# Kernel optimization log

Hardware: AMD Instinct MI355X
Metric: run time of the kernel (lower is better)

## Reference

```python
import jax, jax.numpy as jnp
import numpy as np

D_MODEL = 1024
H = 16
DH = 64
EPS = 1e-5


def _layernorm(x, g, b):
    mu = jnp.mean(x, axis=-1, keepdims=True)
    var = jnp.var(x, axis=-1, keepdims=True)
    return (x - mu) * jax.lax.rsqrt(var + EPS) * g + b


def setup_inputs() -> dict:
    key = jax.random.key(0)
    ks = jax.random.split(key, 16)
    B, L = 4, 4096
    s = 0.02
    inp = {
        "x": jax.random.normal(ks[0], (B, L, D_MODEL), jnp.float32),
        "ln1_g": jnp.ones((D_MODEL,), jnp.float32),
        "ln1_b": jnp.zeros((D_MODEL,), jnp.float32),
        "Wq": jax.random.normal(ks[1], (D_MODEL, H * DH), jnp.float32) * s,
        "bq": jnp.zeros((H * DH,), jnp.float32),
        "Wk": jax.random.normal(ks[2], (D_MODEL, H * DH), jnp.float32) * s,
        "bk": jnp.zeros((H * DH,), jnp.float32),
        "Wv": jax.random.normal(ks[3], (D_MODEL, H * DH), jnp.float32) * s,
        "bv": jnp.zeros((H * DH,), jnp.float32),
        "Wg": jax.random.normal(ks[4], (D_MODEL, H * DH), jnp.float32) * s,
        "bg": jnp.zeros((H * DH,), jnp.float32),
        "decay_logit": jnp.zeros((H,), jnp.float32),
        "Wo": jax.random.normal(ks[5], (H * DH, D_MODEL), jnp.float32) * s,
        "bo": jnp.zeros((D_MODEL,), jnp.float32),
        "ln2_g": jnp.ones((D_MODEL,), jnp.float32),
        "ln2_b": jnp.zeros((D_MODEL,), jnp.float32),
        "W1": jax.random.normal(ks[6], (D_MODEL, 4 * D_MODEL), jnp.float32) * s,
        "b1": jnp.zeros((4 * D_MODEL,), jnp.float32),
        "W2": jax.random.normal(ks[7], (4 * D_MODEL, D_MODEL), jnp.float32) * s,
        "b2": jnp.zeros((D_MODEL,), jnp.float32),
    }
    return inp


def reference(x, ln1_g, ln1_b, Wq, bq, Wk, bk, Wv, bv, Wg, bg, decay_logit,
              Wo, bo, ln2_g, ln2_b, W1, b1, W2, b2):
    B, L, _ = x.shape
    y = _layernorm(x, ln1_g, ln1_b)
    # projections -> [L, B, H, DH] (time-major for scan)
    def proj(W, b):
        return (y @ W + b).reshape(B, L, H, DH).transpose(1, 0, 2, 3)
    q = proj(Wq, bq)
    k = proj(Wk, bk)
    v = proj(Wv, bv)
    g = jax.nn.sigmoid(y @ Wg + bg).reshape(B, L, H, DH).transpose(1, 0, 2, 3)
    decay = jax.nn.sigmoid(decay_logit)[None, :, None]  # [1,H,1]
    scale = DH ** -0.5

    def step(state, qkvg):
        q_t, k_t, v_t, g_t = qkvg
        state = decay * state + k_t * v_t          # [B,H,DH]
        out_t = g_t * q_t * state * scale
        return state, out_t

    state0 = jnp.zeros((B, H, DH), x.dtype)
    _, outs = jax.lax.scan(step, state0, (q, k, v, g))  # [L,B,H,DH]
    o = outs.transpose(1, 0, 2, 3).reshape(B, L, H * DH) @ Wo + bo
    x2 = x + o  # dropout is identity (eval / p=0)
    h = _layernorm(x2, ln2_g, ln2_b)
    ff = jax.nn.gelu(h @ W1 + b1, approximate=False) @ W2 + b2
    return x2 + ff
```

## Files before the change

### kernel.cpp

```cpp
#include <hip/hip_runtime.h>
#include <math.h>


#define D_MODEL 1024
#define LSEQ    4096
#define BATCH   4
#define NROWS   (BATCH * LSEQ)
#define HEADS   16
#define DH      64
#define CHUNK   128
#define NCH     (LSEQ / CHUNK)

typedef short  short8  __attribute__((ext_vector_type(8)));
typedef short  short4v __attribute__((ext_vector_type(4)));
typedef float  float4v __attribute__((ext_vector_type(4)));

__device__ inline short f2bf(float f) {
    unsigned u = __float_as_uint(f);
    u += 0x7fffu + ((u >> 16) & 1u);
    return (short)(u >> 16);
}
__device__ inline float bf2f(short s) {
    return __uint_as_float(((unsigned)(unsigned short)s) << 16);
}

__device__ inline void load_lds16(const short* g, short* l) {
    __builtin_amdgcn_global_load_lds(
        (const __attribute__((address_space(1))) void*)g,
        (__attribute__((address_space(3))) void*)l,
        16, 0, 0);
}

__global__ __launch_bounds__(1024) void transpose_f32_bf16(
    const float* __restrict__ in, short* __restrict__ out, int R, int C)
{
    __shared__ float tile[32][33];
    int tx = threadIdx.x, ty = threadIdx.y;
    int r = blockIdx.y * 32 + ty;
    int c = blockIdx.x * 32 + tx;
    tile[ty][tx] = in[(size_t)r * C + c];
    __syncthreads();
    out[(size_t)(blockIdx.x * 32 + ty) * R + blockIdx.y * 32 + tx] =
        f2bf(tile[tx][ty]);
}

__global__ __launch_bounds__(256) void concat_bias(
    const float* __restrict__ bq, const float* __restrict__ bk,
    const float* __restrict__ bv, const float* __restrict__ bg,
    float* __restrict__ out)
{
    int i = blockIdx.x * 256 + threadIdx.x;
    const float* src = (i < 1024) ? bq : (i < 2048) ? bk : (i < 3072) ? bv : bg;
    out[i] = src[i & 1023];
}

__global__ __launch_bounds__(256) void ln_kernel(
    const float* __restrict__ x, const float* __restrict__ g,
    const float* __restrict__ b, short* __restrict__ y)
{
    int row = blockIdx.x;
    int tid = threadIdx.x;
    const float4* xr = (const float4*)(x + (size_t)row * D_MODEL);
    float4 v = xr[tid];
    float s  = v.x + v.y + v.z + v.w;
    float ss = v.x * v.x + v.y * v.y + v.z * v.z + v.w * v.w;
    #pragma unroll
    for (int off = 32; off > 0; off >>= 1) {
        s  += __shfl_down(s, off);
        ss += __shfl_down(ss, off);
    }
    __shared__ float sbuf[8];
    int wv = tid >> 6, ln = tid & 63;
    if (ln == 0) { sbuf[wv] = s; sbuf[4 + wv] = ss; }
    __syncthreads();
    float tot  = sbuf[0] + sbuf[1] + sbuf[2] + sbuf[3];
    float tot2 = sbuf[4] + sbuf[5] + sbuf[6] + sbuf[7];
    float mu  = tot * (1.0f / D_MODEL);
    float var = tot2 * (1.0f / D_MODEL) - mu * mu;
    float rs  = rsqrtf(var + 1e-5f);
    float4 gg = ((const float4*)g)[tid];
    float4 bb = ((const float4*)b)[tid];
    short4v o;
    o.x = f2bf((v.x - mu) * rs * gg.x + bb.x);
    o.y = f2bf((v.y - mu) * rs * gg.y + bb.y);
    o.z = f2bf((v.z - mu) * rs * gg.z + bb.z);
    o.w = f2bf((v.w - mu) * rs * gg.w + bb.w);
    ((short4v*)y)[(size_t)row * 256 + tid] = o;
}

__global__ __launch_bounds__(512, 2) void gemm_bf16(
    const short* __restrict__ A, const short* __restrict__ BT,
    const float* __restrict__ bias, const float* __restrict__ res,
    float* __restrict__ outf, short* __restrict__ outb,
    int M, int N, int K, int mode)
{
    __shared__ short As[2][16384];
    __shared__ short Bs[2][16384];

    const int gx  = gridDim.x;
    const int nwg = gx * gridDim.y;
    const int lin = blockIdx.x + blockIdx.y * gx;
    const int cpx = nwg >> 3;
    const int wg  = (lin & 7) * cpx + (lin >> 3);
    const int bx  = wg % gx;
    const int by  = wg / gx;
    const int row0 = bx * 256;
    const int col0 = by * 256;

    const int tid  = threadIdx.x;
    const int wave = tid >> 6;
    const int lane = tid & 63;
    const int wm   = wave >> 2;
    const int wn   = wave & 3;
    const int lm   = lane & 15;
    const int q    = lane >> 4;
    const int kq0  = ((q ^ (lm & 7)) << 3);

    const int csw = (((tid & 7) ^ ((tid >> 3) & 7)) << 3);
    const short* gA = A  + (size_t)(row0 + (tid >> 3)) * K + csw;
    const short* gB = BT + (size_t)(col0 + (tid >> 3)) * K + csw;
    short* sA = &As[0][0] + tid * 8;
    short* sB = &Bs[0][0] + tid * 8;
    const size_t K64 = (size_t)64 * K;

    float4v acc[8][4];
    #pragma unroll
    for (int i = 0; i < 8; i++)
        #pragma unroll
        for (int j = 0; j < 4; j++)
            acc[i][j] = (float4v)(0.0f);

    const int NT = K >> 6;

    load_lds16(gA,            sA);
    load_lds16(gA +     K64,  sA + 4096);
    load_lds16(gA + 2 * K64,  sA + 8192);
    load_lds16(gA + 3 * K64,  sA + 12288);
    load_lds16(gB,            sB);
    load_lds16(gB +     K64,  sB + 4096);
    load_lds16(gB + 2 * K64,  sB + 8192);
    load_lds16(gB + 3 * K64,  sB + 12288);
    __syncthreads();

    const short* Abase = &As[0][0] + wm * 8192;
    const short* Bbase = &Bs[0][0] + (wn >> 1) * 8192;
    const int aro = lm * 64;
    const int bro = ((wn & 1) * 64 + lm) * 64;

    short8 aF[4][2];
    short8 bF[2][2][2];

#define MFMA8(QR, QC)                                                        \
    _Pragma("unroll")                                                        \
    for (int ks = 0; ks < 2; ks++)                                           \
        _Pragma("unroll")                                                    \
        for (int i = 0; i < 4; i++)                                          \
            _Pragma("unroll")                                                \
            for (int j = 0; j < 2; j++)                                      \
                acc[(QR) * 4 + i][(QC) * 2 + j] =                            \
                    __builtin_amdgcn_mfma_f32_16x16x32_bf16(                 \
                        aF[i][ks], bF[QC][j][ks],                            \
                        acc[(QR) * 4 + i][(QC) * 2 + j], 0, 0, 0);

    for (int t = 0; t < NT; ++t) {
        const int bufo = (t & 1) << 14;
        const short* Ab = Abase + bufo;
        const short* Bb = Bbase + bufo;
        const int  kb = (t + 1) << 6;
        const bool pf = (t + 1 < NT);
        const int  pfo = ((t + 1) & 1) << 14;

        #pragma unroll
        for (int i = 0; i < 4; i++) {
            const int ar = aro + (i * 16) * 64;
            aF[i][0] = *(const short8*)&Ab[ar + kq0];
            aF[i][1] = *(const short8*)&Ab[ar + (kq0 ^ 32)];
        }
        #pragma unroll
        for (int j = 0; j < 2; j++) {
            const int br = bro + (j * 16) * 64;
            bF[0][j][0] = *(const short8*)&Bb[br + kq0];
            bF[0][j][1] = *(const short8*)&Bb[br + (kq0 ^ 32)];
        }
        if (pf) {
            short* d = sA + pfo;
            load_lds16(gA + kb,            d);
            load_lds16(gA +     K64 + kb,  d + 4096);
            load_lds16(gA + 2 * K64 + kb,  d + 8192);
            load_lds16(gA + 3 * K64 + kb,  d + 12288);
        }
        __builtin_amdgcn_s_barrier();
        __builtin_amdgcn_s_setprio(1);
        MFMA8(0, 0)
        __builtin_amdgcn_s_setprio(0);
        __builtin_amdgcn_s_barrier();

        #pragma unroll
        for (int j = 0; j < 2; j++) {
            const int br = bro + (32 + j * 16) * 64;
            bF[1][j][0] = *(const short8*)&Bb[br + kq0];
            bF[1][j][1] = *(const short8*)&Bb[br + (kq0 ^ 32)];
        }
        if (pf) {
            short* d = sB + pfo;
            load_lds16(gB + kb,            d);
            load_lds16(gB +     K64 + kb,  d + 4096);
            load_lds16(gB + 2 * K64 + kb,  d + 8192);
            load_lds16(gB + 3 * K64 + kb,  d + 12288);
        }
        __builtin_amdgcn_s_barrier();
        __builtin_amdgcn_s_setprio(1);
        MFMA8(0, 1)
        __builtin_amdgcn_s_setprio(0);
        __builtin_amdgcn_s_barrier();

        #pragma unroll
        for (int i = 0; i < 4; i++) {
            const int ar = aro + (64 + i * 16) * 64;
            aF[i][0] = *(const short8*)&Ab[ar + kq0];
            aF[i][1] = *(const short8*)&Ab[ar + (kq0 ^ 32)];
        }
        __builtin_amdgcn_s_barrier();
        __builtin_amdgcn_s_setprio(1);
        MFMA8(1, 0)
        __builtin_amdgcn_s_setprio(0);
        __builtin_amdgcn_s_barrier();

        __builtin_amdgcn_s_setprio(1);
        MFMA8(1, 1)
        __builtin_amdgcn_s_setprio(0);
        __syncthreads();
    }
#undef MFMA8

    const int r4 = q << 2;
    #pragma unroll
    for (int ai = 0; ai < 8; ai++) {
        const int rowg = row0 + wm * 128 + (ai >> 2) * 64 + (ai & 3) * 16 + r4;
        #pragma unroll
        for (int bj = 0; bj < 4; bj++) {
            const int colg = col0 + wn * 64 + (bj >> 1) * 32 + (bj & 1) * 16 + lm;
            const float bcol = bias[colg];
            #pragma unroll
            for (int r2 = 0; r2 < 4; r2++) {
                size_t idx = (size_t)(rowg + r2) * N + colg;
                float v = acc[ai][bj][r2] + bcol;
                if (mode == 0) {
                    if (colg >= 3072) v = 1.0f / (1.0f + expf(-v));
                    outb[idx] = f2bf(v);
                } else if (mode == 1) {
                    outf[idx] = v + res[idx];
                } else {
                    v = 0.5f * v * (1.0f + erff(v * 0.70710678118654752f));
                    outb[idx] = f2bf(v);
                }
            }
        }
    }
}

__global__ __launch_bounds__(256) void scan_pass1(
    const short* __restrict__ qkvg, const float* __restrict__ dlogit,
    float* __restrict__ carry)
{
    int j  = blockIdx.x >> 4;
    int c  = ((blockIdx.x & 15) << 8) + threadIdx.x;
    int b  = c >> 10;
    int col = c & 1023;
    float decay = 1.0f / (1.0f + expf(-dlogit[col >> 6]));
    size_t base = ((size_t)b * LSEQ + j * CHUNK) * 4096 + col;
    float s = 0.0f;
    for (int t = 0; t < CHUNK; ++t) {
        float kk = bf2f(qkvg[base + 1024]);
        float vv = bf2f(qkvg[base + 2048]);
        s = decay * s + kk * vv;
        base += 4096;
    }
    carry[j * 4096 + c] = s;
}

__global__ __launch_bounds__(256) void scan_combine(
    const float* __restrict__ carry, const float* __restrict__ dlogit,
    float* __restrict__ sinit)
{
    int c = blockIdx.x * 256 + threadIdx.x;
    float decay = 1.0f / (1.0f + expf(-dlogit[(c & 1023) >> 6]));
    float dp = powf(decay, (float)CHUNK);
    float s = 0.0f;
    for (int j = 0; j < NCH; ++j) {
        sinit[j * 4096 + c] = s;
        s = dp * s + carry[j * 4096 + c];
    }
}

__global__ __launch_bounds__(256) void scan_pass2(
    const short* __restrict__ qkvg, const float* __restrict__ dlogit,
    const float* __restrict__ sinit, short* __restrict__ att)
{
    int j  = blockIdx.x >> 4;
    int c  = ((blockIdx.x & 15) << 8) + threadIdx.x;
    int b  = c >> 10;
    int col = c & 1023;
    float decay = 1.0f / (1.0f + expf(-dlogit[col >> 6]));
    float s = sinit[j * 4096 + c];
    size_t base  = ((size_t)b * LSEQ + j * CHUNK) * 4096 + col;
    size_t obase = ((size_t)b * LSEQ + j * CHUNK) * 1024 + col;
    for (int t = 0; t < CHUNK; ++t) {
        float qq = bf2f(qkvg[base]);
        float kk = bf2f(qkvg[base + 1024]);
        float vv = bf2f(qkvg[base + 2048]);
        float gg = bf2f(qkvg[base + 3072]);
        s = decay * s + kk * vv;
        att[obase] = f2bf(gg * qq * s * 0.125f);
        base += 4096; obase += 1024;
    }
}

extern "C" void kernel_launch(void* const* d_in, const int* in_sizes, int n_in,
                              void* d_out, int out_size, void* d_ws, size_t ws_size,
                              hipStream_t stream)
{
    const float* x      = (const float*)d_in[0];
    const float* ln1_g  = (const float*)d_in[1];
    const float* ln1_b  = (const float*)d_in[2];
    const float* Wq     = (const float*)d_in[3];
    const float* bq     = (const float*)d_in[4];
    const float* Wk     = (const float*)d_in[5];
    const float* bk     = (const float*)d_in[6];
    const float* Wv     = (const float*)d_in[7];
    const float* bv     = (const float*)d_in[8];
    const float* Wg     = (const float*)d_in[9];
    const float* bg     = (const float*)d_in[10];
    const float* dlog   = (const float*)d_in[11];
    const float* Wo     = (const float*)d_in[12];
    const float* bo     = (const float*)d_in[13];
    const float* ln2_g  = (const float*)d_in[14];
    const float* ln2_b  = (const float*)d_in[15];
    const float* W1     = (const float*)d_in[16];
    const float* b1     = (const float*)d_in[17];
    const float* W2     = (const float*)d_in[18];
    const float* b2     = (const float*)d_in[19];
    float* out = (float*)d_out;

    char* ws = (char*)d_ws;
    size_t off = 0;
    auto alloc = [&](size_t bytes) -> void* {
        void* p = ws + off;
        off += (bytes + 255) & ~(size_t)255;
        return p;
    };
    short* WqkvgT = (short*)alloc((size_t)4096 * 1024 * 2);
    short* WoT    = (short*)alloc((size_t)1024 * 1024 * 2);
    short* W1T    = (short*)alloc((size_t)4096 * 1024 * 2);
    short* W2T    = (short*)alloc((size_t)1024 * 4096 * 2);
    float* biasq  = (float*)alloc((size_t)4096 * 4);
    float* carry  = (float*)alloc((size_t)NCH * 4096 * 4);
    float* sinit  = (float*)alloc((size_t)NCH * 4096 * 4);
    short* bufA   = (short*)alloc((size_t)NROWS * 1024 * 2);
    short* bufB   = (short*)alloc((size_t)NROWS * 4096 * 2);
    float* x2 = out;
    short* ybuf = bufA;
    short* att  = bufA;
    short* hbuf = bufA;
    short* qkvg = bufB;
    short* ff1  = bufB;
    (void)in_sizes; (void)n_in; (void)out_size;

    if (off > ws_size) return;

    dim3 tb(32, 32);
    transpose_f32_bf16<<<dim3(32, 32), tb, 0, stream>>>(Wq, WqkvgT + 0 * 1024 * 1024, 1024, 1024);
    transpose_f32_bf16<<<dim3(32, 32), tb, 0, stream>>>(Wk, WqkvgT + 1 * 1024 * 1024, 1024, 1024);
    transpose_f32_bf16<<<dim3(32, 32), tb, 0, stream>>>(Wv, WqkvgT + 2 * 1024 * 1024, 1024, 1024);
    transpose_f32_bf16<<<dim3(32, 32), tb, 0, stream>>>(Wg, WqkvgT + 3 * 1024 * 1024, 1024, 1024);
    transpose_f32_bf16<<<dim3(32, 32), tb, 0, stream>>>(Wo, WoT, 1024, 1024);
    transpose_f32_bf16<<<dim3(128, 32), tb, 0, stream>>>(W1, W1T, 1024, 4096);
    transpose_f32_bf16<<<dim3(32, 128), tb, 0, stream>>>(W2, W2T, 4096, 1024);
    concat_bias<<<16, 256, 0, stream>>>(bq, bk, bv, bg, biasq);

    ln_kernel<<<NROWS, 256, 0, stream>>>(x, ln1_g, ln1_b, ybuf);

    gemm_bf16<<<dim3(64, 16), 512, 0, stream>>>(
        ybuf, WqkvgT, biasq, nullptr, nullptr, qkvg, NROWS, 4096, 1024, 0);

    scan_pass1 <<<NCH * 16, 256, 0, stream>>>(qkvg, dlog, carry);
    scan_combine<<<16, 256, 0, stream>>>(carry, dlog, sinit);
    scan_pass2 <<<NCH * 16, 256, 0, stream>>>(qkvg, dlog, sinit, att);

    gemm_bf16<<<dim3(64, 4), 512, 0, stream>>>(
        att, WoT, bo, x, x2, nullptr, NROWS, 1024, 1024, 1);

    ln_kernel<<<NROWS, 256, 0, stream>>>(x2, ln2_g, ln2_b, hbuf);

    gemm_bf16<<<dim3(64, 16), 512, 0, stream>>>(
        hbuf, W1T, b1, nullptr, nullptr, ff1, NROWS, 4096, 1024, 2);

    gemm_bf16<<<dim3(64, 4), 512, 0, stream>>>(
        ff1, W2T, b2, x2, out, nullptr, NROWS, 1024, 4096, 1);
}
```

Baseline: 1.034 ms.

## Issue next-tile LDS prefetch at loop top with explicit vmcnt waits

The GEMM main loop now issues all eight global-to-LDS loads for the next K tile at the start of each iteration. It then waits with a partial s_waitcnt vmcnt(8), so only the current tile's loads must have landed, and drops the full __syncthreads at the top and end of the loop. This is meant to give the loads more time in flight and replace the heavyweight syncs with a raw s_barrier. It depends on exact vmcnt counting and on the existing mid-loop barriers keeping the double buffer safe, so any other outstanding vector memory op could break correctness.

New measurement: 1.167 ms. +12.8%, slower.

```diff
diff --git a/kernel.cpp b/kernel.cpp
--- a/kernel.cpp
+++ b/kernel.cpp
@@ -140,7 +140,6 @@
     load_lds16(gB +     K64,  sB + 4096);
     load_lds16(gB + 2 * K64,  sB + 8192);
     load_lds16(gB + 3 * K64,  sB + 12288);
-    __syncthreads();
 
     const short* Abase = &As[0][0] + wm * 8192;
     const short* Bbase = &Bs[0][0] + (wn >> 1) * 8192;
@@ -166,9 +165,29 @@
         const int bufo = (t & 1) << 14;
         const short* Ab = Abase + bufo;
         const short* Bb = Bbase + bufo;
-        const int  kb = (t + 1) << 6;
-        const bool pf = (t + 1 < NT);
-        const int  pfo = ((t + 1) & 1) << 14;
+
+        if (t + 1 < NT) {
+            const int kb  = (t + 1) << 6;
+            const int pfo = ((t + 1) & 1) << 14;
+            short* dA = sA + pfo;
+            short* dB = sB + pfo;
+            load_lds16(gA + kb,            dA);
+            load_lds16(gA +     K64 + kb,  dA + 4096);
+            load_lds16(gA + 2 * K64 + kb,  dA + 8192);
+            load_lds16(gA + 3 * K64 + kb,  dA + 12288);
+            load_lds16(gB + kb,            dB);
+            load_lds16(gB +     K64 + kb,  dB + 4096);
+            load_lds16(gB + 2 * K64 + kb,  dB + 8192);
+            load_lds16(gB + 3 * K64 + kb,  dB + 12288);
+            __builtin_amdgcn_sched_barrier(0);
+            asm volatile("s_waitcnt vmcnt(8)" ::: "memory");
+        } else {
+            __builtin_amdgcn_sched_barrier(0);
+            asm volatile("s_waitcnt vmcnt(0)" ::: "memory");
+        }
+        __builtin_amdgcn_sched_barrier(0);
+        __builtin_amdgcn_s_barrier();
+        __builtin_amdgcn_sched_barrier(0);
 
         #pragma unroll
         for (int i = 0; i < 4; i++) {
@@ -182,13 +201,6 @@
             bF[0][j][0] = *(const short8*)&Bb[br + kq0];
             bF[0][j][1] = *(const short8*)&Bb[br + (kq0 ^ 32)];
         }
-        if (pf) {
-            short* d = sA + pfo;
-            load_lds16(gA + kb,            d);
-            load_lds16(gA +     K64 + kb,  d + 4096);
-            load_lds16(gA + 2 * K64 + kb,  d + 8192);
-            load_lds16(gA + 3 * K64 + kb,  d + 12288);
-        }
         __builtin_amdgcn_s_barrier();
         __builtin_amdgcn_s_setprio(1);
         MFMA8(0, 0)
@@ -201,13 +213,6 @@
             bF[1][j][0] = *(const short8*)&Bb[br + kq0];
             bF[1][j][1] = *(const short8*)&Bb[br + (kq0 ^ 32)];
         }
-        if (pf) {
-            short* d = sB + pfo;
-            load_lds16(gB + kb,            d);
-            load_lds16(gB +     K64 + kb,  d + 4096);
-            load_lds16(gB + 2 * K64 + kb,  d + 8192);
-            load_lds16(gB + 3 * K64 + kb,  d + 12288);
-        }
         __builtin_amdgcn_s_barrier();
         __builtin_amdgcn_s_setprio(1);
         MFMA8(0, 1)
@@ -229,7 +234,6 @@
         __builtin_amdgcn_s_setprio(1);
         MFMA8(1, 1)
         __builtin_amdgcn_s_setprio(0);
-        __syncthreads();
     }
 #undef MFMA8
 
```

## Deepen GEMM global-to-LDS prefetch to two tiles ahead with fine-grained vmcnt waits

Applied to the files above, without the earlier changes.

Restructures the bf16 GEMM main loop so global-to-LDS loads are issued up to two K-tiles ahead. Each quarter-buffer is refilled as soon as its MFMA phase has consumed it, and explicit s_waitcnt vmcnt counts replace the full __syncthreads at the end of each iteration. The loop is unrolled by two over the double buffer. This is meant to hide more global latency and remove the end-of-iteration full-barrier stall. The cost is more in-flight loads, a subtler buffer-reuse ordering, and a loop that assumes NT is even.

New measurement: 1.563 ms. +51.1%, slower.

```diff
diff --git a/kernel.cpp b/kernel.cpp
--- a/kernel.cpp
+++ b/kernel.cpp
@@ -119,8 +119,8 @@
     const int csw = (((tid & 7) ^ ((tid >> 3) & 7)) << 3);
     const short* gA = A  + (size_t)(row0 + (tid >> 3)) * K + csw;
     const short* gB = BT + (size_t)(col0 + (tid >> 3)) * K + csw;
-    short* sA = &As[0][0] + tid * 8;
-    short* sB = &Bs[0][0] + tid * 8;
+    short* stA = &As[0][0] + tid * 8;
+    short* stB = &Bs[0][0] + tid * 8;
     const size_t K64 = (size_t)64 * K;
 
     float4v acc[8][4];
@@ -132,18 +132,6 @@
 
     const int NT = K >> 6;
 
-    load_lds16(gA,            sA);
-    load_lds16(gA +     K64,  sA + 4096);
-    load_lds16(gA + 2 * K64,  sA + 8192);
-    load_lds16(gA + 3 * K64,  sA + 12288);
-    load_lds16(gB,            sB);
-    load_lds16(gB +     K64,  sB + 4096);
-    load_lds16(gB + 2 * K64,  sB + 8192);
-    load_lds16(gB + 3 * K64,  sB + 12288);
-    __syncthreads();
-
-    const short* Abase = &As[0][0] + wm * 8192;
-    const short* Bbase = &Bs[0][0] + (wn >> 1) * 8192;
     const int aro = lm * 64;
     const int bro = ((wn & 1) * 64 + lm) * 64;
 
@@ -162,76 +150,94 @@
                         aF[i][ks], bF[QC][j][ks],                            \
                         acc[(QR) * 4 + i][(QC) * 2 + j], 0, 0, 0);
 
-    for (int t = 0; t < NT; ++t) {
-        const int bufo = (t & 1) << 14;
-        const short* Ab = Abase + bufo;
-        const short* Bb = Bbase + bufo;
-        const int  kb = (t + 1) << 6;
-        const bool pf = (t + 1 < NT);
-        const int  pfo = ((t + 1) & 1) << 14;
-
-        #pragma unroll
-        for (int i = 0; i < 4; i++) {
-            const int ar = aro + (i * 16) * 64;
-            aF[i][0] = *(const short8*)&Ab[ar + kq0];
-            aF[i][1] = *(const short8*)&Ab[ar + (kq0 ^ 32)];
-        }
-        #pragma unroll
-        for (int j = 0; j < 2; j++) {
-            const int br = bro + (j * 16) * 64;
-            bF[0][j][0] = *(const short8*)&Bb[br + kq0];
-            bF[0][j][1] = *(const short8*)&Bb[br + (kq0 ^ 32)];
-        }
-        if (pf) {
-            short* d = sA + pfo;
-            load_lds16(gA + kb,            d);
-            load_lds16(gA +     K64 + kb,  d + 4096);
-            load_lds16(gA + 2 * K64 + kb,  d + 8192);
-            load_lds16(gA + 3 * K64 + kb,  d + 12288);
-        }
-        __builtin_amdgcn_s_barrier();
-        __builtin_amdgcn_s_setprio(1);
-        MFMA8(0, 0)
-        __builtin_amdgcn_s_setprio(0);
-        __builtin_amdgcn_s_barrier();
-
-        #pragma unroll
-        for (int j = 0; j < 2; j++) {
-            const int br = bro + (32 + j * 16) * 64;
-            bF[1][j][0] = *(const short8*)&Bb[br + kq0];
-            bF[1][j][1] = *(const short8*)&Bb[br + (kq0 ^ 32)];
-        }
-        if (pf) {
-            short* d = sB + pfo;
-            load_lds16(gB + kb,            d);
-            load_lds16(gB +     K64 + kb,  d + 4096);
-            load_lds16(gB + 2 * K64 + kb,  d + 8192);
-            load_lds16(gB + 3 * K64 + kb,  d + 12288);
-        }
-        __builtin_amdgcn_s_barrier();
-        __builtin_amdgcn_s_setprio(1);
-        MFMA8(0, 1)
-        __builtin_amdgcn_s_setprio(0);
-        __builtin_amdgcn_s_barrier();
-
-        #pragma unroll
-        for (int i = 0; i < 4; i++) {
-            const int ar = aro + (64 + i * 16) * 64;
-            aF[i][0] = *(const short8*)&Ab[ar + kq0];
-            aF[i][1] = *(const short8*)&Ab[ar + (kq0 ^ 32)];
-        }
-        __builtin_amdgcn_s_barrier();
-        __builtin_amdgcn_s_setprio(1);
-        MFMA8(1, 0)
-        __builtin_amdgcn_s_setprio(0);
-        __builtin_amdgcn_s_barrier();
-
-        __builtin_amdgcn_s_setprio(1);
-        MFMA8(1, 1)
-        __builtin_amdgcn_s_setprio(0);
-        __syncthreads();
-    }
+#define DS_A_QR(Ab, QR)                                                      \
+    _Pragma("unroll")                                                        \
+    for (int i = 0; i < 4; i++) {                                            \
+        const int ar = aro + ((QR) * 64 + i * 16) * 64;                      \
+        aF[i][0] = *(const short8*)&(Ab)[ar + kq0];                          \
+        aF[i][1] = *(const short8*)&(Ab)[ar + (kq0 ^ 32)];                   \
+    }
+
+#define DS_B_QC(Bb, QC)                                                      \
+    _Pragma("unroll")                                                        \
+    for (int j = 0; j < 2; j++) {                                            \
+        const int br = bro + ((QC) * 32 + j * 16) * 64;                      \
+        bF[QC][j][0] = *(const short8*)&(Bb)[br + kq0];                      \
+        bF[QC][j][1] = *(const short8*)&(Bb)[br + (kq0 ^ 32)];               \
+    }
+
+#define BAR __builtin_amdgcn_s_barrier()
+#define PRIO1 __builtin_amdgcn_s_setprio(1)
+#define PRIO0 __builtin_amdgcn_s_setprio(0)
+
+    load_lds16(gA,                stA);
+    load_lds16(gA + 2 * K64,      stA + 8192);
+    load_lds16(gB,                stB);
+    load_lds16(gB + 2 * K64,      stB + 8192);
+    load_lds16(gA + K64,          stA + 4096);
+    load_lds16(gA + 3 * K64,      stA + 12288);
+    load_lds16(gB + K64,          stB + 4096);
+    load_lds16(gB + 3 * K64,      stB + 12288);
+    load_lds16(gA + 64,           stA + 16384);
+    load_lds16(gA + 2 * K64 + 64, stA + 16384 + 8192);
+    load_lds16(gB + 64,           stB + 16384);
+    load_lds16(gB + 2 * K64 + 64, stB + 16384 + 8192);
+    load_lds16(gA + K64 + 64,     stA + 16384 + 4096);
+    load_lds16(gA + 3 * K64 + 64, stA + 16384 + 12288);
+    asm volatile("s_waitcnt vmcnt(6)" ::: "memory");
+    BAR;
+
+#define BLOCK(T, CUR)                                                        \
+    {                                                                        \
+        const short* Ab = &As[0][0] + (CUR) + wm * 8192;                     \
+        const short* Bb = &Bs[0][0] + (CUR) + (wn >> 1) * 8192;              \
+        const int kb1 = ((T) + 1) << 6;                                      \
+        const int kb2 = ((T) + 2) << 6;                                      \
+        const bool p1ok = (T) + 1 < NT, p2ok = (T) + 2 < NT;                 \
+              \
+        DS_A_QR(Ab, 0)                                                       \
+        DS_B_QC(Bb, 0)                                                       \
+        if (p1ok) {                                                          \
+            load_lds16(gB + K64 + kb1,     stB + ((CUR) ^ 16384) + 4096);    \
+            load_lds16(gB + 3 * K64 + kb1, stB + ((CUR) ^ 16384) + 12288);   \
+        }                                                                    \
+        BAR; PRIO1; MFMA8(0, 0) PRIO0; BAR;                                  \
+                      \
+        DS_B_QC(Bb, 1)                                                       \
+        if (p2ok) {                                                          \
+            load_lds16(gA + kb2,           stA + (CUR));                     \
+            load_lds16(gA + 2 * K64 + kb2, stA + (CUR) + 8192);              \
+        }                                                                    \
+        BAR; PRIO1; MFMA8(0, 1) PRIO0; BAR;                                  \
+                                  \
+        DS_A_QR(Ab, 1)                                                       \
+        if (p2ok) {                                                          \
+            load_lds16(gB + kb2,           stB + (CUR));                     \
+            load_lds16(gB + 2 * K64 + kb2, stB + (CUR) + 8192);              \
+        }                                                                    \
+        BAR; PRIO1; MFMA8(1, 0) PRIO0; BAR;                                  \
+                       \
+        if (p2ok) {                                                          \
+            load_lds16(gA + K64 + kb2,     stA + (CUR) + 4096);              \
+            load_lds16(gA + 3 * K64 + kb2, stA + (CUR) + 12288);             \
+            asm volatile("s_waitcnt vmcnt(6)" ::: "memory");                 \
+        } else if (p1ok) {                                                   \
+            asm volatile("s_waitcnt vmcnt(0)" ::: "memory");                 \
+        }                                                                    \
+        BAR; PRIO1; MFMA8(1, 1) PRIO0; BAR;                                  \
+    }
+
+    for (int t = 0; t < NT; t += 2) {
+        BLOCK(t,     0)
+        BLOCK(t + 1, 16384)
+    }
+#undef BLOCK
 #undef MFMA8
+#undef DS_A_QR
+#undef DS_B_QC
+#undef BAR
+#undef PRIO1
+#undef PRIO0
 
     const int r4 = q << 2;
     #pragma unroll
```
